# Performance work log

Hardware: AMD Instinct MI355X
Metric: run time of the kernel (lower is better)

The kernel has to match this reference:

```python
import jax, jax.numpy as jnp
import numpy as np
import math

HIDDEN = 4096
N_HEADS = 32
N_KV_HEADS = 8
HEAD_DIM = HIDDEN // N_HEADS  # 128
N_GROUPS = N_HEADS // N_KV_HEADS  # 4
ROPE_THETA = 10000.0


def setup_inputs() -> dict:
    key = jax.random.key(0)
    ks = jax.random.split(key, 5)
    B, S = 2, 2048
    hidden_states = jax.random.normal(ks[0], (B, S, HIDDEN), dtype=jnp.float32)
    position_ids = jnp.broadcast_to(jnp.arange(S, dtype=jnp.int32)[None, :], (B, S))
    sc = 1.0 / math.sqrt(HIDDEN)
    Wq = jax.random.normal(ks[1], (HIDDEN, N_HEADS * HEAD_DIM), dtype=jnp.float32) * sc
    Wk = jax.random.normal(ks[2], (HIDDEN, N_KV_HEADS * HEAD_DIM), dtype=jnp.float32) * sc
    Wv = jax.random.normal(ks[3], (HIDDEN, N_KV_HEADS * HEAD_DIM), dtype=jnp.float32) * sc
    Wo = jax.random.normal(ks[4], (HIDDEN, HIDDEN), dtype=jnp.float32) * sc
    return {"hidden_states": hidden_states, "position_ids": position_ids,
            "Wq": Wq, "Wk": Wk, "Wv": Wv, "Wo": Wo}


def _rope_cos_sin(position_ids):
    # inv_freq: [head_dim//2]
    inv_freq = 1.0 / (ROPE_THETA ** (jnp.arange(0, HEAD_DIM, 2, dtype=jnp.float32) / HEAD_DIM))
    freqs = position_ids.astype(jnp.float32)[..., None] * inv_freq  # [B, S, hd/2]
    emb = jnp.concatenate([freqs, freqs], axis=-1)  # [B, S, hd]
    return jnp.cos(emb), jnp.sin(emb)


def _rotate_half(x):
    h = x.shape[-1] // 2
    return jnp.concatenate([-x[..., h:], x[..., :h]], axis=-1)


def _apply_rope(x, cos, sin):
    # x: [B, H, S, hd]; cos/sin: [B, S, hd] -> unsqueeze head dim
    return x * cos[:, None] + _rotate_half(x) * sin[:, None]


def reference(hidden_states, position_ids, Wq, Wk, Wv, Wo):
    B, S, _ = hidden_states.shape
    q = (hidden_states @ Wq).reshape(B, S, N_HEADS, HEAD_DIM).transpose(0, 2, 1, 3)
    k = (hidden_states @ Wk).reshape(B, S, N_KV_HEADS, HEAD_DIM).transpose(0, 2, 1, 3)
    v = (hidden_states @ Wv).reshape(B, S, N_KV_HEADS, HEAD_DIM).transpose(0, 2, 1, 3)

    cos, sin = _rope_cos_sin(position_ids)
    q = _apply_rope(q, cos, sin)
    k = _apply_rope(k, cos, sin)

    # repeat_kv: (B, kvH, S, d) -> (B, H, S, d)
    k = jnp.repeat(k, N_GROUPS, axis=1)
    v = jnp.repeat(v, N_GROUPS, axis=1)

    scores = jnp.einsum('bhqd,bhkd->bhqk', q, k) / math.sqrt(HEAD_DIM)
    causal = jnp.tril(jnp.ones((S, S), dtype=bool))
    neg = jnp.finfo(jnp.float32).min
    scores = jnp.where(causal[None, None], scores, neg)
    attn = jax.nn.softmax(scores.astype(jnp.float32), axis=-1).astype(q.dtype)

    out = jnp.einsum('bhqk,bhkd->bhqd', attn, v)
    out = out.transpose(0, 2, 1, 3).reshape(B, S, HIDDEN)
    return out @ Wo
```

## Files before the change

kernel.cpp:

```cpp
#include <hip/hip_runtime.h>
#include <hip/hip_bf16.h>
#include <math.h>

#define HIDDEN 4096
#define NH 32
#define NKV 8
#define HD 128
#define S_LEN 2048
#define BATCH 2
#define MROWS (BATCH * S_LEN)
#define QKVW 6144

typedef __attribute__((ext_vector_type(8))) __bf16 bf16x8;
typedef __attribute__((ext_vector_type(4))) float f32x4;

__device__ __forceinline__ f32x4 mfma16(bf16x8 a, bf16x8 b, f32x4 c) {
  return __builtin_amdgcn_mfma_f32_16x16x32_bf16(a, b, c, 0, 0, 0);
}

__device__ __forceinline__ void gload16(const __bf16* g, const __bf16* l) {
  __builtin_amdgcn_global_load_lds(
      (const __attribute__((address_space(1))) void*)g,
      (__attribute__((address_space(3))) void*)l, 16, 0, 0);
}

#define SBAR()                          \
  do {                                  \
    __builtin_amdgcn_sched_barrier(0);  \
    __builtin_amdgcn_s_barrier();       \
    __builtin_amdgcn_sched_barrier(0);  \
  } while (0)

#define VMCNT8()                                              \
  do {                                                        \
    __builtin_amdgcn_sched_barrier(0);                        \
    asm volatile("s_waitcnt vmcnt(8)" ::: "memory");          \
  } while (0)

#define VMCNT6()                                              \
  do {                                                        \
    __builtin_amdgcn_sched_barrier(0);                        \
    asm volatile("s_waitcnt vmcnt(6)" ::: "memory");          \
  } while (0)

__global__ __launch_bounds__(256) void cvt_kernel(const float* __restrict__ in,
                                                  __bf16* __restrict__ out, int n) {
  int i = (blockIdx.x * 256 + threadIdx.x) * 8;
  if (i >= n) return;
  float4 a = *reinterpret_cast<const float4*>(in + i);
  float4 b = *reinterpret_cast<const float4*>(in + i + 4);
  bf16x8 t;
  t[0] = (__bf16)a.x; t[1] = (__bf16)a.y; t[2] = (__bf16)a.z; t[3] = (__bf16)a.w;
  t[4] = (__bf16)b.x; t[5] = (__bf16)b.y; t[6] = (__bf16)b.z; t[7] = (__bf16)b.w;
  *reinterpret_cast<bf16x8*>(out + i) = t;
}

__global__ __launch_bounds__(256) void tcvt3_kernel(const float* __restrict__ Wq,
                                                    const float* __restrict__ Wk,
                                                    const float* __restrict__ Wv,
                                                    __bf16* __restrict__ Wt) {
  __shared__ float t[32][33];
  int z = blockIdx.z;
  const float* in;
  __bf16* out;
  int C;
  if (z == 0)      { in = Wq; out = Wt;                         C = 4096; }
  else if (z == 1) { in = Wk; out = Wt + (size_t)4096 * 4096;   C = 1024; }
  else             { in = Wv; out = Wt + (size_t)5120 * 4096;   C = 1024; }
  if ((int)blockIdx.x * 32 >= C) return;
  int tx = threadIdx.x, ty = threadIdx.y;
  int r0 = blockIdx.y * 32, c0 = blockIdx.x * 32;
#pragma unroll
  for (int i = 0; i < 4; i++)
    t[ty + i * 8][tx] = in[(size_t)(r0 + ty + i * 8) * C + c0 + tx];
  __syncthreads();
#pragma unroll
  for (int i = 0; i < 4; i++)
    out[(size_t)(c0 + ty + i * 8) * 4096 + r0 + tx] = (__bf16)t[tx][ty + i * 8];
}

__global__ __launch_bounds__(256) void tcvt_f32(const float* __restrict__ in,
                                                __bf16* __restrict__ out,
                                                int R, int C) {
  __shared__ float t[32][33];
  int tx = threadIdx.x, ty = threadIdx.y;
  int r0 = blockIdx.y * 32, c0 = blockIdx.x * 32;
#pragma unroll
  for (int i = 0; i < 4; i++)
    t[ty + i * 8][tx] = in[(size_t)(r0 + ty + i * 8) * C + c0 + tx];
  __syncthreads();
#pragma unroll
  for (int i = 0; i < 4; i++)
    out[(size_t)(c0 + ty + i * 8) * R + r0 + tx] = (__bf16)t[tx][ty + i * 8];
}

__global__ __launch_bounds__(256) void tvt_kernel(const __bf16* __restrict__ qkv,
                                                  __bf16* __restrict__ vt) {
  __shared__ __bf16 t[32][33];
  int tx = threadIdx.x, ty = threadIdx.y;
  int z = blockIdx.z;
  int b = z >> 3, kvh = z & 7;
  int kv0 = blockIdx.y * 32, d0 = blockIdx.x * 32;
#pragma unroll
  for (int i = 0; i < 4; i++)
    t[ty + i * 8][tx] =
        qkv[(size_t)(b * S_LEN + kv0 + ty + i * 8) * QKVW + 5120 + kvh * HD + d0 + tx];
  __syncthreads();
  int cperm = kv0 + 2 * (tx & 15) + (tx >> 4);
#pragma unroll
  for (int i = 0; i < 4; i++)
    vt[((size_t)z * HD + d0 + ty + i * 8) * S_LEN + cperm] = t[tx][ty + i * 8];
}

template<typename CT>
__global__ __launch_bounds__(512, 2) void gemm256(const __bf16* __restrict__ A,
                                                  const __bf16* __restrict__ Bt,
                                                  CT* __restrict__ C,
                                                  int K, int ldc, int nbx) {
  __shared__ char lds[131072];
  const int tid = threadIdx.x;
  const int l = tid & 63, w = tid >> 6;
  const int lrow = l & 15, lg = l >> 4;
  const int sw = (lrow & 7) << 4;

  int nwg = gridDim.x;
  int swz = (blockIdx.x & 7) * (nwg >> 3) + (blockIdx.x >> 3);
  int bx = swz % nbx, by = swz / nbx;
  int m0 = by * 256, n0 = bx * 256;

  const int rA = w * 8 + (l >> 3);
  const int csw = ((l & 7) ^ (l >> 3)) * 8;
  const __bf16* As_[2][2];
  const __bf16* Bs_[2][2];
#pragma unroll
  for (int h = 0; h < 2; h++)
#pragma unroll
    for (int p = 0; p < 2; p++) {
      As_[h][p] = A + (size_t)(m0 + h * 128 + p * 64 + rA) * K + csw;
      Bs_[h][p] = Bt + (size_t)(n0 + h * 128 + p * 64 + rA) * K + csw;
    }

  auto stageA = [&](int par, int h, int kt) {
#pragma unroll
    for (int p = 0; p < 2; p++)
      gload16(As_[h][p] + kt * 64,
              (const __bf16*)(lds + par * 32768 + h * 16384 + p * 8192 + w * 1024));
  };
  auto stageB = [&](int par, int h, int kt) {
#pragma unroll
    for (int p = 0; p < 2; p++)
      gload16(Bs_[h][p] + kt * 64,
              (const __bf16*)(lds + 65536 + par * 32768 + h * 16384 + p * 8192 + w * 1024));
  };

  const int arbase = (w >> 2) * 64 + lrow;
  const int brbase = (w & 3) * 32 + lrow;

  bf16x8 aA[4][2];
  bf16x8 bB[2][2][2];

  auto readA = [&](int par, int ah) {
#pragma unroll
    for (int i = 0; i < 4; i++)
#pragma unroll
      for (int kk = 0; kk < 2; kk++)
        aA[i][kk] = *reinterpret_cast<const bf16x8*>(
            lds + par * 32768 + (arbase + i * 16 + ah * 128) * 128 +
            ((kk * 64 + lg * 16) ^ sw));
  };
  auto readB = [&](int par, int bh) {
#pragma unroll
    for (int j = 0; j < 2; j++)
#pragma unroll
      for (int kk = 0; kk < 2; kk++)
        bB[bh][j][kk] = *reinterpret_cast<const bf16x8*>(
            lds + 65536 + par * 32768 + (brbase + j * 16 + bh * 128) * 128 +
            ((kk * 64 + lg * 16) ^ sw));
  };

  f32x4 acc[8][4];
#pragma unroll
  for (int i = 0; i < 8; i++)
#pragma unroll
    for (int j = 0; j < 4; j++) {
      acc[i][j][0] = 0.f; acc[i][j][1] = 0.f; acc[i][j][2] = 0.f; acc[i][j][3] = 0.f;
    }

  const int NT = K >> 6;

  stageA(0, 0, 0); stageB(0, 0, 0);
  stageA(0, 1, 0); stageB(0, 1, 0);
  stageA(1, 0, 1); stageB(1, 0, 1);
  VMCNT8();
  SBAR();

#define MFMA_QUAD(AH, BH)                                                   \
  __builtin_amdgcn_s_setprio(1);                                            \
  _Pragma("unroll") for (int i4 = 0; i4 < 4; i4++)                          \
      _Pragma("unroll") for (int j2 = 0; j2 < 2; j2++)                      \
          _Pragma("unroll") for (int kk = 0; kk < 2; kk++)                  \
              acc[(AH)*4 + i4][(BH)*2 + j2] =                               \
                  mfma16(aA[i4][kk], bB[BH][j2][kk], acc[(AH)*4 + i4][(BH)*2 + j2]); \
  __builtin_amdgcn_s_setprio(0);

#define GTILE256(PAR, TT)                                                   \
  {                                                                         \
    const int t1n = ((TT) + 1 < NT) ? (TT) + 1 : 0;                         \
    const int t2n = ((TT) + 2 < NT) ? (TT) + 2 : 0;                         \
    readA(PAR, 0);                                                          \
    readB(PAR, 0);                                                          \
    stageA(PAR ^ 1, 1, t1n);                                                \
    stageB(PAR ^ 1, 1, t1n);                                                \
    VMCNT8();                                                               \
    SBAR();                                                                 \
    MFMA_QUAD(0, 0);                                                        \
    SBAR();                                                                 \
    readB(PAR, 1);                                                          \
    stageA(PAR, 0, t2n);                                                    \
    SBAR();                                                                 \
    MFMA_QUAD(0, 1);                                                        \
    SBAR();                                                                 \
    readA(PAR, 1);                                                          \
    stageB(PAR, 0, t2n);                                                    \
    SBAR();                                                                 \
    MFMA_QUAD(1, 0);                                                        \
    MFMA_QUAD(1, 1);                                                        \
    VMCNT8();                                                               \
    SBAR();                                                                 \
  }

  for (int t = 0; t < NT; t += 2) {
    GTILE256(0, t);
    GTILE256(1, t + 1);
  }
#undef GTILE256
#undef MFMA_QUAD

#pragma unroll
  for (int i = 0; i < 8; i++) {
    int row = m0 + (w >> 2) * 64 + (i & 3) * 16 + (i >> 2) * 128 + lg * 4;
#pragma unroll
    for (int j = 0; j < 4; j++) {
      int col = n0 + (w & 3) * 32 + (j & 1) * 16 + (j >> 1) * 128 + lrow;
#pragma unroll
      for (int jj = 0; jj < 4; jj++)
        C[(size_t)(row + jj) * ldc + col] = (CT)acc[i][j][jj];
    }
  }
}

template<typename CT>
__global__ __launch_bounds__(512, 2) void gemm128(const __bf16* __restrict__ A,
                                                  const __bf16* __restrict__ Bt,
                                                  CT* __restrict__ C,
                                                  int K, int ldc, int nbx) {
  __shared__ char lds[98304];
  const int tid = threadIdx.x;
  const int l = tid & 63, w = tid >> 6;
  const int lrow = l & 15, lg = l >> 4;
  const int sw = (lrow & 7) << 4;

  int nwg = gridDim.x;
  int swz = (blockIdx.x & 7) * (nwg >> 3) + (blockIdx.x >> 3);
  int bx = swz % nbx, by = swz / nbx;
  int m0 = by * 256, n0 = bx * 128;

  const int rA = w * 8 + (l >> 3);
  const int csw = ((l & 7) ^ (l >> 3)) * 8;
  const __bf16* As_[2][2];
  const __bf16* Bs_[2];
#pragma unroll
  for (int h = 0; h < 2; h++)
#pragma unroll
    for (int p = 0; p < 2; p++)
      As_[h][p] = A + (size_t)(m0 + h * 128 + p * 64 + rA) * K + csw;
#pragma unroll
  for (int p = 0; p < 2; p++)
    Bs_[p] = Bt + (size_t)(n0 + p * 64 + rA) * K + csw;

  auto stageA = [&](int par, int h, int kt) {
#pragma unroll
    for (int p = 0; p < 2; p++)
      gload16(As_[h][p] + kt * 64,
              (const __bf16*)(lds + par * 32768 + h * 16384 + p * 8192 + w * 1024));
  };
  auto stageB = [&](int par, int kt) {
#pragma unroll
    for (int p = 0; p < 2; p++)
      gload16(Bs_[p] + kt * 64,
              (const __bf16*)(lds + 65536 + par * 16384 + p * 8192 + w * 1024));
  };

  const int arbase = (w >> 2) * 64 + lrow;
  const int brbase = (w & 3) * 32 + lrow;

  bf16x8 aA[4][2];
  bf16x8 bB[2][2];

  auto readA = [&](int par, int ah) {
#pragma unroll
    for (int i = 0; i < 4; i++)
#pragma unroll
      for (int kk = 0; kk < 2; kk++)
        aA[i][kk] = *reinterpret_cast<const bf16x8*>(
            lds + par * 32768 + (arbase + i * 16 + ah * 128) * 128 +
            ((kk * 64 + lg * 16) ^ sw));
  };
  auto readB = [&](int par) {
#pragma unroll
    for (int j = 0; j < 2; j++)
#pragma unroll
      for (int kk = 0; kk < 2; kk++)
        bB[j][kk] = *reinterpret_cast<const bf16x8*>(
            lds + 65536 + par * 16384 + (brbase + j * 16) * 128 +
            ((kk * 64 + lg * 16) ^ sw));
  };

  f32x4 acc[8][2];
#pragma unroll
  for (int i = 0; i < 8; i++)
#pragma unroll
    for (int j = 0; j < 2; j++) {
      acc[i][j][0] = 0.f; acc[i][j][1] = 0.f; acc[i][j][2] = 0.f; acc[i][j][3] = 0.f;
    }

  const int NT = K >> 6;

  stageA(0, 0, 0); stageB(0, 0);
  stageA(0, 1, 0); stageB(1, 1); stageA(1, 0, 1);
  VMCNT6();
  SBAR();

#define MFMA_HALF(AH)                                                        \
  __builtin_amdgcn_s_setprio(1);                                             \
  _Pragma("unroll") for (int i4 = 0; i4 < 4; i4++)                           \
      _Pragma("unroll") for (int j2 = 0; j2 < 2; j2++)                       \
          _Pragma("unroll") for (int kk = 0; kk < 2; kk++)                   \
              acc[(AH)*4 + i4][j2] =                                         \
                  mfma16(aA[i4][kk], bB[j2][kk], acc[(AH)*4 + i4][j2]);      \
  __builtin_amdgcn_s_setprio(0);

#define GTILE128(PAR, TT)                                                    \
  {                                                                          \
    const int t1n = ((TT) + 1 < NT) ? (TT) + 1 : 0;                          \
    const int t2n = ((TT) + 2 < NT) ? (TT) + 2 : 0;                          \
    readA(PAR, 0);                                                           \
    readB(PAR);                                                              \
    stageA(PAR ^ 1, 1, t1n);                                                 \
    VMCNT6();                                                                \
    SBAR();                                                                  \
    MFMA_HALF(0);                                                            \
    SBAR();                                                                  \
    readA(PAR, 1);                                                           \
    stageB(PAR, t2n);                                                        \
    stageA(PAR, 0, t2n);                                                     \
    SBAR();                                                                  \
    MFMA_HALF(1);                                                            \
    VMCNT6();                                                                \
    SBAR();                                                                  \
  }

  for (int t = 0; t < NT; t += 2) {
    GTILE128(0, t);
    GTILE128(1, t + 1);
  }
#undef GTILE128
#undef MFMA_HALF

#pragma unroll
  for (int i = 0; i < 8; i++) {
    int row = m0 + (w >> 2) * 64 + (i & 3) * 16 + (i >> 2) * 128 + lg * 4;
#pragma unroll
    for (int j = 0; j < 2; j++) {
      int col = n0 + (w & 3) * 32 + j * 16 + lrow;
#pragma unroll
      for (int jj = 0; jj < 4; jj++)
        C[(size_t)(row + jj) * ldc + col] = (CT)acc[i][j][jj];
    }
  }
}

__global__ __launch_bounds__(256) void rope_kernel(__bf16* __restrict__ qkv,
                                                   const int* __restrict__ pos) {
  int row = blockIdx.x;
  int t = threadIdx.x;
  float p = (float)pos[row];
  __bf16* rbase = qkv + (size_t)row * QKVW;

  {
    int head = t >> 3, chunk = t & 7;
    __bf16* base = rbase + head * HD + chunk * 8;
    bf16x8 x1 = *reinterpret_cast<const bf16x8*>(base);
    bf16x8 x2 = *reinterpret_cast<const bf16x8*>(base + 64);
    bf16x8 o1, o2;
#pragma unroll
    for (int e = 0; e < 8; e++) {
      float ang = p * exp2f(-0.20762050f * (float)(chunk * 8 + e));
      float s, c;
      __sincosf(ang, &s, &c);
      float a = (float)x1[e], b2 = (float)x2[e];
      o1[e] = (__bf16)(a * c - b2 * s);
      o2[e] = (__bf16)(b2 * c + a * s);
    }
    *reinterpret_cast<bf16x8*>(base) = o1;
    *reinterpret_cast<bf16x8*>(base + 64) = o2;
  }
  if (t < 64) {
    int head = t >> 3, chunk = t & 7;
    __bf16* base = rbase + 4096 + head * HD + chunk * 8;
    bf16x8 x1 = *reinterpret_cast<const bf16x8*>(base);
    bf16x8 x2 = *reinterpret_cast<const bf16x8*>(base + 64);
    bf16x8 o1, o2;
#pragma unroll
    for (int e = 0; e < 8; e++) {
      float ang = p * exp2f(-0.20762050f * (float)(chunk * 8 + e));
      float s, c;
      __sincosf(ang, &s, &c);
      float a = (float)x1[e], b2 = (float)x2[e];
      o1[e] = (__bf16)(a * c - b2 * s);
      o2[e] = (__bf16)(b2 * c + a * s);
    }
    *reinterpret_cast<bf16x8*>(base) = o1;
    *reinterpret_cast<bf16x8*>(base + 64) = o2;
  }
}

__global__ __launch_bounds__(512) void attn_kernel(const __bf16* __restrict__ qkv,
                                                   const __bf16* __restrict__ vt,
                                                   __bf16* __restrict__ out) {
  __shared__ __bf16 Ks[64 * 128];
  __shared__ __bf16 Vs[128 * 64];
  __shared__ __bf16 Ps[8][32][68];

  int tid = threadIdx.x;
  int l = tid & 63, w = tid >> 6;
  int bid = blockIdx.x;
  int qblk = 7 - (bid >> 6);
  int rem = bid & 63;
  int h = rem & 31, b = rem >> 5;
  int kvh = h >> 2;
  int q0w = qblk * 256 + w * 32;
  int lrow = l & 15, lg = l >> 4;
  int sw = (lrow & 7) << 4;
  const float SCL = 0.08838834764831845f * 1.4426950408889634f;

  const __bf16* kbase = qkv + (size_t)(b * S_LEN) * QKVW + 4096 + kvh * HD;
  const __bf16* vbase = vt + ((size_t)(b * NKV + kvh) * HD) * S_LEN;

  int krow = tid >> 3;
  int kslot = (tid & 7) * 2;
  int vrow = tid >> 2;
  int vslot = (tid & 3) * 2;
  char* KsB = (char*)Ks;
  char* VsB = (char*)Vs;
  int koff0 = krow * 256 + ((kslot * 16) ^ ((krow & 7) << 4));
  int koff1 = krow * 256 + (((kslot + 1) * 16) ^ ((krow & 7) << 4));
  int voff0 = vrow * 128 + ((vslot * 16) ^ ((vrow & 7) << 4));
  int voff1 = vrow * 128 + (((vslot + 1) * 16) ^ ((vrow & 7) << 4));
  const __bf16* kg = kbase + (size_t)krow * QKVW + kslot * 8;
  const __bf16* vg = vbase + (size_t)vrow * S_LEN + vslot * 8;

  bf16x8 qf[2][4];
#pragma unroll
  for (int mi = 0; mi < 2; mi++) {
    const __bf16* qp = qkv + (size_t)(b * S_LEN + q0w + mi * 16 + lrow) * QKVW + h * HD + lg * 8;
#pragma unroll
    for (int kk = 0; kk < 4; kk++) {
      bf16x8 t = *reinterpret_cast<const bf16x8*>(qp + kk * 32);
#pragma unroll
      for (int e = 0; e < 8; e++) t[e] = (__bf16)((float)t[e] * SCL);
      qf[mi][kk] = t;
    }
  }

  f32x4 ov[2][8];
#pragma unroll
  for (int mi = 0; mi < 2; mi++)
#pragma unroll
    for (int n = 0; n < 8; n++) {
      ov[mi][n][0] = 0.f; ov[mi][n][1] = 0.f; ov[mi][n][2] = 0.f; ov[mi][n][3] = 0.f;
    }
  float m[2][4], ssum[2][4];
#pragma unroll
  for (int mi = 0; mi < 2; mi++)
#pragma unroll
    for (int jj = 0; jj < 4; jj++) { m[mi][jj] = -3.0e38f; ssum[mi][jj] = 0.f; }

  int nt = 4 * qblk + 4;
  bf16x8 kr0, kr1, vr0, vr1;

  kr0 = *reinterpret_cast<const bf16x8*>(kg);
  kr1 = *reinterpret_cast<const bf16x8*>(kg + 8);
  vr0 = *reinterpret_cast<const bf16x8*>(vg);
  vr1 = *reinterpret_cast<const bf16x8*>(vg + 8);
  *reinterpret_cast<bf16x8*>(KsB + koff0) = kr0;
  *reinterpret_cast<bf16x8*>(KsB + koff1) = kr1;
  *reinterpret_cast<bf16x8*>(VsB + voff0) = vr0;
  *reinterpret_cast<bf16x8*>(VsB + voff1) = vr1;
  __syncthreads();

  for (int t = 0;; t++) {
    int kv0 = t * 64;
    bool more = (t + 1 < nt);
    if (more) {
      int kvn = kv0 + 64;
      kr0 = *reinterpret_cast<const bf16x8*>(kg + (size_t)kvn * QKVW);
      kr1 = *reinterpret_cast<const bf16x8*>(kg + (size_t)kvn * QKVW + 8);
      vr0 = *reinterpret_cast<const bf16x8*>(vg + kvn);
      vr1 = *reinterpret_cast<const bf16x8*>(vg + kvn + 8);
    }

    bool active = (kv0 <= q0w + 31);
    if (active) {
      f32x4 sc[2][4];
#pragma unroll
      for (int mi = 0; mi < 2; mi++)
#pragma unroll
        for (int c = 0; c < 4; c++) {
          sc[mi][c][0] = 0.f; sc[mi][c][1] = 0.f; sc[mi][c][2] = 0.f; sc[mi][c][3] = 0.f;
        }
#pragma unroll
      for (int c = 0; c < 4; c++) {
        int rb = (c * 16 + lrow) * 256;
#pragma unroll
        for (int kk = 0; kk < 4; kk++) {
          bf16x8 kf = *reinterpret_cast<const bf16x8*>(KsB + rb + ((kk * 64 + lg * 16) ^ sw));
          sc[0][c] = mfma16(qf[0][kk], kf, sc[0][c]);
          sc[1][c] = mfma16(qf[1][kk], kf, sc[1][c]);
        }
      }

      bool bound = (kv0 + 64 > q0w);
      if (bound) {
#pragma unroll
        for (int mi = 0; mi < 2; mi++)
#pragma unroll
          for (int jj = 0; jj < 4; jj++) {
            int qidx = q0w + mi * 16 + lg * 4 + jj;
            if (kv0 + lrow > qidx)      sc[mi][0][jj] = -3.0e38f;
            if (kv0 + 16 + lrow > qidx) sc[mi][1][jj] = -3.0e38f;
            if (kv0 + 32 + lrow > qidx) sc[mi][2][jj] = -3.0e38f;
            if (kv0 + 48 + lrow > qidx) sc[mi][3][jj] = -3.0e38f;
          }
      }

      float lm[2][4];
      bool lanegrow = false;
#pragma unroll
      for (int mi = 0; mi < 2; mi++)
#pragma unroll
        for (int jj = 0; jj < 4; jj++) {
          lm[mi][jj] = fmaxf(fmaxf(sc[mi][0][jj], sc[mi][1][jj]),
                             fmaxf(sc[mi][2][jj], sc[mi][3][jj]));
          lanegrow |= (lm[mi][jj] > m[mi][jj] + 8.0f);
        }

      if (__any(lanegrow)) {
        float es[2][4];
#pragma unroll
        for (int mi = 0; mi < 2; mi++)
#pragma unroll
          for (int jj = 0; jj < 4; jj++) {
            float r = lm[mi][jj];
            r = fmaxf(r, __shfl_xor(r, 1));
            r = fmaxf(r, __shfl_xor(r, 2));
            r = fmaxf(r, __shfl_xor(r, 4));
            r = fmaxf(r, __shfl_xor(r, 8));
            float mo = m[mi][jj];
            bool grow = (r > mo + 8.0f);
            float mn = grow ? r : mo;
            float e = grow ? exp2f(mo - r) : 1.0f;
            es[mi][jj] = e;
            m[mi][jj] = mn;
            ssum[mi][jj] *= e;
          }
#pragma unroll
        for (int mi = 0; mi < 2; mi++)
#pragma unroll
          for (int n = 0; n < 8; n++)
#pragma unroll
            for (int jj = 0; jj < 4; jj++) ov[mi][n][jj] *= es[mi][jj];
      }

#pragma unroll
      for (int mi = 0; mi < 2; mi++)
#pragma unroll
        for (int jj = 0; jj < 4; jj++) {
          float mn = m[mi][jj];
          float p0 = exp2f(sc[mi][0][jj] - mn), p1 = exp2f(sc[mi][1][jj] - mn);
          float p2 = exp2f(sc[mi][2][jj] - mn), p3 = exp2f(sc[mi][3][jj] - mn);
          ssum[mi][jj] += (p0 + p1) + (p2 + p3);
          int pr = mi * 16 + lg * 4 + jj;
          union { __bf16 hh[2]; unsigned int u; } a01, a23;
          a01.hh[0] = (__bf16)p0; a01.hh[1] = (__bf16)p1;
          a23.hh[0] = (__bf16)p2; a23.hh[1] = (__bf16)p3;
          *reinterpret_cast<unsigned int*>(&Ps[w][pr][2 * lrow]) = a01.u;
          *reinterpret_cast<unsigned int*>(&Ps[w][pr][32 + 2 * lrow]) = a23.u;
        }

#pragma unroll
      for (int kvs = 0; kvs < 2; kvs++) {
        bf16x8 pf0 = *reinterpret_cast<const bf16x8*>(&Ps[w][lrow][kvs * 32 + lg * 8]);
        bf16x8 pf1 = *reinterpret_cast<const bf16x8*>(&Ps[w][16 + lrow][kvs * 32 + lg * 8]);
#pragma unroll
        for (int n = 0; n < 8; n++) {
          bf16x8 vf = *reinterpret_cast<const bf16x8*>(
              VsB + (n * 16 + lrow) * 128 + ((kvs * 64 + lg * 16) ^ sw));
          ov[0][n] = mfma16(pf0, vf, ov[0][n]);
          ov[1][n] = mfma16(pf1, vf, ov[1][n]);
        }
      }
    }

    if (!more) break;
    __syncthreads();
    *reinterpret_cast<bf16x8*>(KsB + koff0) = kr0;
    *reinterpret_cast<bf16x8*>(KsB + koff1) = kr1;
    *reinterpret_cast<bf16x8*>(VsB + voff0) = vr0;
    *reinterpret_cast<bf16x8*>(VsB + voff1) = vr1;
    __syncthreads();
  }

  float rinv[2][4];
#pragma unroll
  for (int mi = 0; mi < 2; mi++)
#pragma unroll
    for (int jj = 0; jj < 4; jj++) {
      float s = ssum[mi][jj];
      s += __shfl_xor(s, 1);
      s += __shfl_xor(s, 2);
      s += __shfl_xor(s, 4);
      s += __shfl_xor(s, 8);
      rinv[mi][jj] = 1.0f / s;
    }
#pragma unroll
  for (int mi = 0; mi < 2; mi++)
#pragma unroll
    for (int n = 0; n < 8; n++)
#pragma unroll
      for (int jj = 0; jj < 4; jj++) {
        out[(size_t)(b * S_LEN + q0w + mi * 16 + lg * 4 + jj) * HIDDEN + h * HD + n * 16 + lrow] =
            (__bf16)(ov[mi][n][jj] * rinv[mi][jj]);
      }
}

extern "C" void kernel_launch(void* const* d_in, const int* in_sizes, int n_in,
                              void* d_out, int out_size, void* d_ws, size_t ws_size,
                              hipStream_t stream) {
  const float* hidden = (const float*)d_in[0];
  const int* posids   = (const int*)d_in[1];
  const float* Wq     = (const float*)d_in[2];
  const float* Wk     = (const float*)d_in[3];
  const float* Wv     = (const float*)d_in[4];
  const float* Wo     = (const float*)d_in[5];
  float* out = (float*)d_out;

  char* ws = (char*)d_ws;
  __bf16* h_bf    = (__bf16*)(ws + 0);
  __bf16* a_buf   = h_bf;
  __bf16* Wt      = (__bf16*)(ws + 33554432);
  __bf16* qkv_buf = (__bf16*)(ws + 83886080);
  __bf16* vt_buf  = (__bf16*)(ws + 134217728);

  dim3 b256(256), b328(32, 8), b512(512);

  cvt_kernel<<<dim3(MROWS * HIDDEN / (256 * 8)), b256, 0, stream>>>(hidden, h_bf, MROWS * HIDDEN);

  tcvt3_kernel<<<dim3(128, 128, 3), b328, 0, stream>>>(Wq, Wk, Wv, Wt);

  gemm256<__bf16><<<dim3(256), b512, 0, stream>>>(
      h_bf, Wt, qkv_buf, HIDDEN, QKVW, 4096 / 256);
  gemm128<__bf16><<<dim3(256), b512, 0, stream>>>(
      h_bf, Wt + (size_t)4096 * 4096, qkv_buf + 4096, HIDDEN, QKVW, 2048 / 128);

  rope_kernel<<<dim3(MROWS), b256, 0, stream>>>(qkv_buf, posids);

  tvt_kernel<<<dim3(HD / 32, S_LEN / 32, BATCH * NKV), b328, 0, stream>>>(qkv_buf, vt_buf);

  attn_kernel<<<dim3(8 * NH * BATCH), b512, 0, stream>>>(qkv_buf, vt_buf, a_buf);

  tcvt_f32<<<dim3(HIDDEN / 32, HIDDEN / 32), b328, 0, stream>>>(Wo, Wt, HIDDEN, HIDDEN);

  gemm256<float><<<dim3(256), b512, 0, stream>>>(
      a_buf, Wt, out, HIDDEN, HIDDEN, HIDDEN / 256);
}
```

Before: 468.2 us.

## Compute transposed S tile to keep P in registers, drop LDS P staging

The QK^T MFMA now swaps its operands so each lane holds scores for one query row across several KV columns. The probabilities can then be packed straight into bf16x8 A-operands for the PV MFMA, with no round trip through LDS. This removes the shared-memory P buffer, its writes and reads, and shrinks the row-max and row-sum shuffles to two steps. In exchange it adds lane broadcasts to move the rescale factors and normalizers into the output layout. Launch bounds also now request 4 blocks per CU, which caps registers per thread and risks spills.

After: 847.7 us. 81.1% more time.

```diff
diff --git a/kernel.cpp b/kernel.cpp
--- a/kernel.cpp
+++ b/kernel.cpp
@@ -425,12 +425,11 @@
   }
 }
 
-__global__ __launch_bounds__(512) void attn_kernel(const __bf16* __restrict__ qkv,
-                                                   const __bf16* __restrict__ vt,
-                                                   __bf16* __restrict__ out) {
+__global__ __launch_bounds__(512, 4) void attn_kernel(const __bf16* __restrict__ qkv,
+                                                      const __bf16* __restrict__ vt,
+                                                      __bf16* __restrict__ out) {
   __shared__ __bf16 Ks[64 * 128];
   __shared__ __bf16 Vs[128 * 64];
-  __shared__ __bf16 Ps[8][32][68];
 
   int tid = threadIdx.x;
   int l = tid & 63, w = tid >> 6;
@@ -480,11 +479,9 @@
     for (int n = 0; n < 8; n++) {
       ov[mi][n][0] = 0.f; ov[mi][n][1] = 0.f; ov[mi][n][2] = 0.f; ov[mi][n][3] = 0.f;
     }
-  float m[2][4], ssum[2][4];
-#pragma unroll
-  for (int mi = 0; mi < 2; mi++)
-#pragma unroll
-    for (int jj = 0; jj < 4; jj++) { m[mi][jj] = -3.0e38f; ssum[mi][jj] = 0.f; }
+  float m[2], ssum[2];
+  m[0] = -3.0e38f; m[1] = -3.0e38f;
+  ssum[0] = 0.f; ssum[1] = 0.f;
 
   int nt = 4 * qblk + 4;
   bf16x8 kr0, kr1, vr0, vr1;
@@ -525,89 +522,90 @@
 #pragma unroll
         for (int kk = 0; kk < 4; kk++) {
           bf16x8 kf = *reinterpret_cast<const bf16x8*>(KsB + rb + ((kk * 64 + lg * 16) ^ sw));
-          sc[0][c] = mfma16(qf[0][kk], kf, sc[0][c]);
-          sc[1][c] = mfma16(qf[1][kk], kf, sc[1][c]);
+          sc[0][c] = mfma16(kf, qf[0][kk], sc[0][c]);
+          sc[1][c] = mfma16(kf, qf[1][kk], sc[1][c]);
         }
       }
 
       bool bound = (kv0 + 64 > q0w);
       if (bound) {
 #pragma unroll
+        for (int mi = 0; mi < 2; mi++) {
+          int qidx = q0w + mi * 16 + lrow;
+#pragma unroll
+          for (int jj = 0; jj < 4; jj++) {
+            int kvb = kv0 + lg * 4 + jj;
+            if (kvb > qidx)      sc[mi][0][jj] = -3.0e38f;
+            if (kvb + 16 > qidx) sc[mi][1][jj] = -3.0e38f;
+            if (kvb + 32 > qidx) sc[mi][2][jj] = -3.0e38f;
+            if (kvb + 48 > qidx) sc[mi][3][jj] = -3.0e38f;
+          }
+        }
+      }
+
+      float lm[2];
+      bool lanegrow = false;
+#pragma unroll
+      for (int mi = 0; mi < 2; mi++) {
+        float a0 = fmaxf(fmaxf(sc[mi][0][0], sc[mi][0][1]), fmaxf(sc[mi][0][2], sc[mi][0][3]));
+        float a1 = fmaxf(fmaxf(sc[mi][1][0], sc[mi][1][1]), fmaxf(sc[mi][1][2], sc[mi][1][3]));
+        float a2 = fmaxf(fmaxf(sc[mi][2][0], sc[mi][2][1]), fmaxf(sc[mi][2][2], sc[mi][2][3]));
+        float a3 = fmaxf(fmaxf(sc[mi][3][0], sc[mi][3][1]), fmaxf(sc[mi][3][2], sc[mi][3][3]));
+        lm[mi] = fmaxf(fmaxf(a0, a1), fmaxf(a2, a3));
+        lanegrow |= (lm[mi] > m[mi] + 8.0f);
+      }
+
+      if (__any(lanegrow)) {
+        float es[2];
+#pragma unroll
+        for (int mi = 0; mi < 2; mi++) {
+          float r = lm[mi];
+          r = fmaxf(r, __shfl_xor(r, 16));
+          r = fmaxf(r, __shfl_xor(r, 32));
+          float mo = m[mi];
+          bool grow = (r > mo + 8.0f);
+          float mn = grow ? r : mo;
+          float e = grow ? exp2f(mo - r) : 1.0f;
+          es[mi] = e;
+          m[mi] = mn;
+          ssum[mi] *= e;
+        }
+        float esv[2][4];
+#pragma unroll
         for (int mi = 0; mi < 2; mi++)
 #pragma unroll
-          for (int jj = 0; jj < 4; jj++) {
-            int qidx = q0w + mi * 16 + lg * 4 + jj;
-            if (kv0 + lrow > qidx)      sc[mi][0][jj] = -3.0e38f;
-            if (kv0 + 16 + lrow > qidx) sc[mi][1][jj] = -3.0e38f;
-            if (kv0 + 32 + lrow > qidx) sc[mi][2][jj] = -3.0e38f;
-            if (kv0 + 48 + lrow > qidx) sc[mi][3][jj] = -3.0e38f;
+          for (int jj = 0; jj < 4; jj++)
+            esv[mi][jj] = __shfl(es[mi], lg * 4 + jj);
+#pragma unroll
+        for (int mi = 0; mi < 2; mi++)
+#pragma unroll
+          for (int n = 0; n < 8; n++)
+#pragma unroll
+            for (int jj = 0; jj < 4; jj++) ov[mi][n][jj] *= esv[mi][jj];
+      }
+
+      bf16x8 pa[2][2];
+#pragma unroll
+      for (int mi = 0; mi < 2; mi++) {
+        float mn = m[mi];
+#pragma unroll
+        for (int c = 0; c < 4; c++)
+#pragma unroll
+          for (int r = 0; r < 4; r++) {
+            float p = exp2f(sc[mi][c][r] - mn);
+            ssum[mi] += p;
+            pa[mi][c >> 1][(r << 1) | (c & 1)] = (__bf16)p;
           }
       }
 
-      float lm[2][4];
-      bool lanegrow = false;
-#pragma unroll
-      for (int mi = 0; mi < 2; mi++)
-#pragma unroll
-        for (int jj = 0; jj < 4; jj++) {
-          lm[mi][jj] = fmaxf(fmaxf(sc[mi][0][jj], sc[mi][1][jj]),
-                             fmaxf(sc[mi][2][jj], sc[mi][3][jj]));
-          lanegrow |= (lm[mi][jj] > m[mi][jj] + 8.0f);
-        }
-
-      if (__any(lanegrow)) {
-        float es[2][4];
-#pragma unroll
-        for (int mi = 0; mi < 2; mi++)
-#pragma unroll
-          for (int jj = 0; jj < 4; jj++) {
-            float r = lm[mi][jj];
-            r = fmaxf(r, __shfl_xor(r, 1));
-            r = fmaxf(r, __shfl_xor(r, 2));
-            r = fmaxf(r, __shfl_xor(r, 4));
-            r = fmaxf(r, __shfl_xor(r, 8));
-            float mo = m[mi][jj];
-            bool grow = (r > mo + 8.0f);
-            float mn = grow ? r : mo;
-            float e = grow ? exp2f(mo - r) : 1.0f;
-            es[mi][jj] = e;
-            m[mi][jj] = mn;
-            ssum[mi][jj] *= e;
-          }
-#pragma unroll
-        for (int mi = 0; mi < 2; mi++)
-#pragma unroll
-          for (int n = 0; n < 8; n++)
-#pragma unroll
-            for (int jj = 0; jj < 4; jj++) ov[mi][n][jj] *= es[mi][jj];
-      }
-
-#pragma unroll
-      for (int mi = 0; mi < 2; mi++)
-#pragma unroll
-        for (int jj = 0; jj < 4; jj++) {
-          float mn = m[mi][jj];
-          float p0 = exp2f(sc[mi][0][jj] - mn), p1 = exp2f(sc[mi][1][jj] - mn);
-          float p2 = exp2f(sc[mi][2][jj] - mn), p3 = exp2f(sc[mi][3][jj] - mn);
-          ssum[mi][jj] += (p0 + p1) + (p2 + p3);
-          int pr = mi * 16 + lg * 4 + jj;
-          union { __bf16 hh[2]; unsigned int u; } a01, a23;
-          a01.hh[0] = (__bf16)p0; a01.hh[1] = (__bf16)p1;
-          a23.hh[0] = (__bf16)p2; a23.hh[1] = (__bf16)p3;
-          *reinterpret_cast<unsigned int*>(&Ps[w][pr][2 * lrow]) = a01.u;
-          *reinterpret_cast<unsigned int*>(&Ps[w][pr][32 + 2 * lrow]) = a23.u;
-        }
-
 #pragma unroll
       for (int kvs = 0; kvs < 2; kvs++) {
-        bf16x8 pf0 = *reinterpret_cast<const bf16x8*>(&Ps[w][lrow][kvs * 32 + lg * 8]);
-        bf16x8 pf1 = *reinterpret_cast<const bf16x8*>(&Ps[w][16 + lrow][kvs * 32 + lg * 8]);
 #pragma unroll
         for (int n = 0; n < 8; n++) {
           bf16x8 vf = *reinterpret_cast<const bf16x8*>(
               VsB + (n * 16 + lrow) * 128 + ((kvs * 64 + lg * 16) ^ sw));
-          ov[0][n] = mfma16(pf0, vf, ov[0][n]);
-          ov[1][n] = mfma16(pf1, vf, ov[1][n]);
+          ov[0][n] = mfma16(pa[0][kvs], vf, ov[0][n]);
+          ov[1][n] = mfma16(pa[1][kvs], vf, ov[1][n]);
         }
       }
     }
@@ -621,18 +619,20 @@
     __syncthreads();
   }
 
+  float rs[2];
+#pragma unroll
+  for (int mi = 0; mi < 2; mi++) {
+    float s = ssum[mi];
+    s += __shfl_xor(s, 16);
+    s += __shfl_xor(s, 32);
+    rs[mi] = s;
+  }
   float rinv[2][4];
 #pragma unroll
   for (int mi = 0; mi < 2; mi++)
 #pragma unroll
-    for (int jj = 0; jj < 4; jj++) {
-      float s = ssum[mi][jj];
-      s += __shfl_xor(s, 1);
-      s += __shfl_xor(s, 2);
-      s += __shfl_xor(s, 4);
-      s += __shfl_xor(s, 8);
-      rinv[mi][jj] = 1.0f / s;
-    }
+    for (int jj = 0; jj < 4; jj++)
+      rinv[mi][jj] = 1.0f / __shfl(rs[mi], lg * 4 + jj);
 #pragma unroll
   for (int mi = 0; mi < 2; mi++)
 #pragma unroll
```
